# Optimization experiments

Measured on AMD Instinct MI355X. Metric: run time of the kernel, lower is better.

Reference implementation:

```python
import jax, jax.numpy as jnp
import numpy as np

B, CIN, H, W = 4, 272, 32, 32
D, NHEAD, DFF, E, TOPK, NDEC = 256, 8, 1024, 8, 2, 2
HW = H * W


def _sine_pos():
    npf = D // 2
    ye = jnp.cumsum(jnp.ones((H, W), jnp.float32), 0)
    xe = jnp.cumsum(jnp.ones((H, W), jnp.float32), 1)
    eps, scale = 1e-6, 2.0 * np.pi
    ye = ye / (ye[-1:, :] + eps) * scale
    xe = xe / (xe[:, -1:] + eps) * scale
    t = jnp.arange(npf, dtype=jnp.float32)
    dim_t = 10000.0 ** (2.0 * jnp.floor(t / 2.0) / npf)
    px = xe[:, :, None] / dim_t
    py = ye[:, :, None] / dim_t
    px = jnp.stack((jnp.sin(px[:, :, 0::2]), jnp.cos(px[:, :, 1::2])), axis=3).reshape(H, W, npf)
    py = jnp.stack((jnp.sin(py[:, :, 0::2]), jnp.cos(py[:, :, 1::2])), axis=3).reshape(H, W, npf)
    return jnp.concatenate((py, px), axis=2).reshape(HW, D)


def _ln(v, g, b):
    m = v.mean(-1, keepdims=True)
    var = ((v - m) ** 2).mean(-1, keepdims=True)
    return (v - m) / jnp.sqrt(var + 1e-5) * g + b


def _mha(q_in, k_in, v_in, Wqkv, bqkv, Wo, bo):
    # seq-first [S,B,D], torch nn.MultiheadAttention math (dropout off)
    S = q_in.shape[0]; T = k_in.shape[0]; dh = D // NHEAD
    Wq, Wk, Wv = jnp.split(Wqkv, 3, 0)
    bq, bk, bv = jnp.split(bqkv, 3)
    q = (q_in @ Wq.T + bq).reshape(S, B, NHEAD, dh)
    k = (k_in @ Wk.T + bk).reshape(T, B, NHEAD, dh)
    v = (v_in @ Wv.T + bv).reshape(T, B, NHEAD, dh)
    attn = jax.nn.softmax(jnp.einsum('sbhd,tbhd->bhst', q, k) / np.sqrt(dh), axis=-1)
    o = jnp.einsum('bhst,tbhd->sbhd', attn, v).reshape(S, B, D)
    return o @ Wo.T + bo


def _moe(xt, Wg, bg, W1, b1, W2, b2):
    # FMoETransformerMLP with NaiveGate: top-k gate, per-expert 2-layer MLP, weighted combine
    S = xt.shape[0]
    xf = xt.reshape(-1, D)
    N = xf.shape[0]
    logits = xf @ Wg.T + bg                              # [N, E]
    topv, topi = jax.lax.top_k(logits, TOPK)             # [N, k]
    score = jax.nn.softmax(topv, axis=-1)                # softmax over selected logits
    comb = jnp.zeros((N, E), xf.dtype).at[jnp.arange(N)[:, None], topi].add(score)
    h = jax.nn.relu(jnp.einsum('nd,edh->neh', xf, W1) + b1)   # [N, E, DFF]
    y = jnp.einsum('neh,ehd->ned', h, W2) + b2                # [N, E, D]
    out = jnp.einsum('ne,ned->nd', comb, y)
    return out.reshape(S, B, D)


def setup_inputs() -> dict:
    key = jax.random.key(0)
    ks = iter(jax.random.split(key, 32))
    g = lambda shp, s=0.02: s * jax.random.normal(next(ks), shp, jnp.float32)
    inp = {
        'x': jax.random.normal(next(ks), (B, CIN, H, W), jnp.float32),
        'Wi': g((D, CIN)), 'bi': jnp.zeros((D,), jnp.float32),
        'learned_embed': g((HW, D), 1.0),
        'Wqkv_s': g((3 * D, D)), 'bqkv_s': jnp.zeros((3 * D,), jnp.float32),
        'Wo_s': g((D, D)), 'bo_s': jnp.zeros((D,), jnp.float32),
        'Wqkv_c': g((3 * D, D)), 'bqkv_c': jnp.zeros((3 * D,), jnp.float32),
        'Wo_c': g((D, D)), 'bo_c': jnp.zeros((D,), jnp.float32),
        'ln_g': jnp.ones((4 * NDEC, D), jnp.float32), 'ln_b': jnp.zeros((4 * NDEC, D), jnp.float32),
        'gate_w1': g((E, D)), 'gate_b1': jnp.zeros((E,), jnp.float32),
        'W1a': g((E, D, DFF)), 'b1a': jnp.zeros((E, DFF), jnp.float32),
        'W2a': g((E, DFF, D)), 'b2a': jnp.zeros((E, D), jnp.float32),
        'gate_w2': g((E, D)), 'gate_b2': jnp.zeros((E,), jnp.float32),
        'W1b': g((E, D, DFF)), 'b1b': jnp.zeros((E, DFF), jnp.float32),
        'W2b': g((E, DFF, D)), 'b2b': jnp.zeros((E, D), jnp.float32),
        'Wout': g((CIN, D)), 'bout': jnp.zeros((CIN,), jnp.float32),
    }
    return inp


def reference(x, Wi, bi, learned_embed, Wqkv_s, bqkv_s, Wo_s, bo_s,
              Wqkv_c, bqkv_c, Wo_c, bo_c, ln_g, ln_b,
              gate_w1, gate_b1, W1a, b1a, W2a, b2a,
              gate_w2, gate_b2, W1b, b1b, W2b, b2b, Wout, bout):
    tokens = x.transpose(2, 3, 0, 1).reshape(HW, B, CIN)   # 'b c h w -> (h w) b c'
    src = tokens @ Wi.T + bi                               # input_proj
    pos = _sine_pos()[:, None, :]                          # [HW,1,D] broadcast over batch
    enc = src
    dec = src
    for i in range(NDEC):
        tgt = jnp.broadcast_to(learned_embed[:, None, :], (HW, B, D))
        t2 = _mha(tgt + pos, enc + pos, enc, Wqkv_s, bqkv_s, Wo_s, bo_s)
        tgt = _ln(tgt + t2, ln_g[4 * i], ln_b[4 * i])
        t2 = _mha(tgt + pos, dec + pos, dec, Wqkv_c, bqkv_c, Wo_c, bo_c)
        tgt = _ln(tgt + t2, ln_g[4 * i + 1], ln_b[4 * i + 1])
        od = tgt + _moe(tgt, gate_w1, gate_b1, W1a, b1a, W2a, b2a)   # post-lnorm: residual only
        od = _ln(od, ln_g[4 * i + 2], ln_b[4 * i + 2])
        od = od + _moe(od, gate_w2, gate_b2, W1b, b1b, W2b, b2b)
        dec = _ln(od, ln_g[4 * i + 3], ln_b[4 * i + 3])
    rec = dec @ Wout.T + bout                              # output_proj, [HW,B,CIN]
    feature_rec = rec.reshape(H, W, B, CIN).transpose(2, 3, 0, 1)
    return feature_rec
```

## Files before the change

### kernel.cpp

```cpp
#include <hip/hip_runtime.h>

#define NHW 1024
#define NB 4
#define DM 256
#define NTOK 4096
#define NCIN 272
#define NDFF 1024

typedef unsigned short u16;
typedef unsigned int u32;
typedef __attribute__((ext_vector_type(8))) short s16x8;
typedef __attribute__((ext_vector_type(4))) float f32x4;

static const int GEMM_SMEM32 = (32+32+64+64)*56*2;

__device__ __forceinline__ float4 ld4(const float* p){ return *(const float4*)p; }
__device__ __forceinline__ void st4(float* p, float4 v){ *(float4*)p = v; }

__device__ __forceinline__ void splitf(float x, u16& h, u16& l){
  u32 u = __float_as_uint(x);
  u32 hu = (u + (0x7FFFu + ((u >> 16) & 1u))) >> 16;
  h = (u16)hu;
  float hf = __uint_as_float(hu << 16);
  float r = x - hf;
  u32 v = __float_as_uint(r);
  v += 0x7FFFu + ((v >> 16) & 1u);
  l = (u16)(v >> 16);
}

__global__ void pos_kernel(float* __restrict__ pos){
  int s = blockIdx.x, d = threadIdx.x;
  int row = s >> 5, col = s & 31;
  float base = (d < 128) ? (float)(row + 1) : (float)(col + 1);
  float val = base / (32.0f + 1e-6f) * 6.2831853071795864f;
  int dd = (d < 128) ? d : d - 128;
  int mf = dd >> 1;
  float f = powf(10000.0f, (float)mf * (1.0f/64.0f));
  float a = val / f;
  pos[s*DM + d] = (dd & 1) ? cosf(a) : sinf(a);
}

__global__ void tin_kernel(const float* __restrict__ x, float* __restrict__ tok){
  int idx = blockIdx.x*256 + threadIdx.x;
  if (idx >= NTOK*NCIN) return;
  int c = idx % NCIN;
  int n = idx / NCIN;
  int s = n >> 2, b = n & 3;
  tok[idx] = x[((long)(b*NCIN + c))*NHW + s];
}
__global__ void tout_kernel(const float* __restrict__ rec, float* __restrict__ out){
  int idx = blockIdx.x*256 + threadIdx.x;
  if (idx >= NTOK*NCIN) return;
  int s = idx & (NHW-1);
  int bc = idx >> 10;
  int b = bc / NCIN, c = bc % NCIN;
  out[idx] = rec[((long)(s*NB + b))*NCIN + c];
}

__global__ __launch_bounds__(256) void tconv_kernel(const float* __restrict__ in,
    u16* __restrict__ oh, u16* __restrict__ ol, int K, int N){
  __shared__ float tile[32][33];
  long base = (long)blockIdx.z * (long)K * (long)N;
  int k0 = blockIdx.y*32, n0 = blockIdx.x*32;
  int tx = threadIdx.x & 31, ty = threadIdx.x >> 5;
  #pragma unroll
  for (int i=0;i<32;i+=8)
    tile[ty+i][tx] = in[base + (long)(k0+ty+i)*N + n0+tx];
  __syncthreads();
  #pragma unroll
  for (int i=0;i<32;i+=8){
    float v = tile[tx][ty+i];
    u16 h,l; splitf(v,h,l);
    long o = base + (long)(n0+ty+i)*K + k0+tx;
    oh[o]=h; ol[o]=l;
  }
}

__global__ void wsplit_kernel(const float* __restrict__ in, u16* __restrict__ oh,
    u16* __restrict__ ol, int n){
  int i = blockIdx.x*256 + threadIdx.x;
  if (i < n){ u16 h,l; splitf(in[i],h,l); oh[i]=h; ol[i]=l; }
}

template<bool GROUPED, bool INDIRECT, int ASRC, bool RELU, int CDST>
__device__ __forceinline__ void sgemm_body(
    const void* __restrict__ Av, int lda,
    const float* __restrict__ pos,
    const u16* __restrict__ Bhp, const u16* __restrict__ Blp, int ldb,
    const float* __restrict__ bias,
    void* __restrict__ Cv, int ldc,
    int M, int N, int K,
    const int* __restrict__ map,
    const int* __restrict__ cnt,
    const int* __restrict__ offs,
    const int* __restrict__ jmap,
    const float* __restrict__ sflat,
    long strideB, int strideBias, int e)
{
  constexpr int BM = 32;
  int rows = GROUPED ? cnt[e] : M;
  int bm = blockIdx.x, bn = blockIdx.y;
  if (bm*BM >= rows) return;
  int row0 = GROUPED ? offs[e] : 0;
  const float* Af = (const float*)Av;
  const u32*   Ap = (const u32*)Av;
  if (GROUPED){ Bhp += (long)e*strideB; Blp += (long)e*strideB; }
  const float* biasp = bias ? (GROUPED ? bias + (long)e*strideBias : bias) : nullptr;

  extern __shared__ u16 smem[];
  u16* Ah = smem;
  u16* Al = Ah + BM*56;
  u16* Bh = Al + BM*56;
  u16* Bl = Bh + 64*56;

  int tid = threadIdx.x;
  int w = tid >> 6, ln = tid & 63;
  int wm = w >> 1, wn = w & 1;
  int lr = ln & 15, lh = ln >> 4;
  int srow = tid >> 2, sseg = tid & 3;

  int bgrow = bn*64 + srow;
  bool bok = bgrow < N;
  int agrow = bm*BM + srow;
  bool aok = (tid < BM*4) && (agrow < rows);
  long arow = 0;
  if (aok) arow = INDIRECT ? (long)map[row0 + agrow] : (long)(row0 + agrow);

  const f32x4 z4 = {0.f,0.f,0.f,0.f};
  f32x4 acc0 = z4, acc1 = z4;
  const s16x8 z8 = {0,0,0,0,0,0,0,0};

  s16x8 rBh = z8, rBl = z8;
  uint4 rA0 = make_uint4(0,0,0,0), rA1 = make_uint4(0,0,0,0);
  float4 rP0 = make_float4(0.f,0.f,0.f,0.f), rP1 = rP0;

  auto load_stage = [&](int k0){
    int kk = k0 + sseg*8;
    bool kok = kk < K;
    rBh = z8; rBl = z8;
    if (bok && kok){
      rBh = *(const s16x8*)&Bhp[(long)bgrow*ldb + kk];
      rBl = *(const s16x8*)&Blp[(long)bgrow*ldb + kk];
    }
    if (tid < BM*4){
      rA0 = make_uint4(0,0,0,0); rA1 = make_uint4(0,0,0,0);
      if (ASRC==2 || ASRC==3){ rP0 = make_float4(0.f,0.f,0.f,0.f); rP1 = rP0; }
      if (aok && kok){
        if (ASRC == 1){
          rA0 = *(const uint4*)&Ap[arow*lda + kk];
          rA1 = *(const uint4*)&Ap[arow*lda + kk + 4];
        } else {
          long aoff = (ASRC==3 ? (long)(arow>>2) : arow)*lda + kk;
          rA0 = *(const uint4*)&Af[aoff];
          rA1 = *(const uint4*)&Af[aoff + 4];
          if (ASRC==2 || ASRC==3){
            long poff = (long)(arow>>2)*DM + kk;
            rP0 = ld4(&pos[poff]);
            rP1 = ld4(&pos[poff + 4]);
          }
        }
      }
    }
  };

  auto write_stage = [&](){
    *(s16x8*)&Bh[srow*56 + sseg*8] = rBh;
    *(s16x8*)&Bl[srow*56 + sseg*8] = rBl;
    if (tid < BM*4){
      s16x8 hv, lv;
      if (ASRC == 1){
        u32 ws[8] = {rA0.x,rA0.y,rA0.z,rA0.w,rA1.x,rA1.y,rA1.z,rA1.w};
        #pragma unroll
        for (int t=0;t<8;t++){ hv[t]=(short)(ws[t]&0xFFFFu); lv[t]=(short)(ws[t]>>16); }
      } else {
        float xs[8] = {__uint_as_float(rA0.x),__uint_as_float(rA0.y),
                       __uint_as_float(rA0.z),__uint_as_float(rA0.w),
                       __uint_as_float(rA1.x),__uint_as_float(rA1.y),
                       __uint_as_float(rA1.z),__uint_as_float(rA1.w)};
        if (ASRC==2 || ASRC==3){
          xs[0]+=rP0.x; xs[1]+=rP0.y; xs[2]+=rP0.z; xs[3]+=rP0.w;
          xs[4]+=rP1.x; xs[5]+=rP1.y; xs[6]+=rP1.z; xs[7]+=rP1.w;
        }
        #pragma unroll
        for (int t=0;t<8;t++){ u16 hh,ll; splitf(xs[t],hh,ll); hv[t]=(short)hh; lv[t]=(short)ll; }
      }
      *(s16x8*)&Ah[srow*56 + sseg*8] = hv;
      *(s16x8*)&Al[srow*56 + sseg*8] = lv;
    }
  };

  load_stage(0);
  for (int k0 = 0; k0 < K; k0 += 32){
    write_stage();
    __syncthreads();
    if (k0 + 32 < K) load_stage(k0 + 32);
    s16x8 a0h = *(const s16x8*)&Ah[(wm*16 + lr)*56 + lh*8];
    s16x8 a0l = *(const s16x8*)&Al[(wm*16 + lr)*56 + lh*8];
    s16x8 b0h = *(const s16x8*)&Bh[(wn*32      + lr)*56 + lh*8];
    s16x8 b1h = *(const s16x8*)&Bh[(wn*32 + 16 + lr)*56 + lh*8];
    s16x8 b0l = *(const s16x8*)&Bl[(wn*32      + lr)*56 + lh*8];
    s16x8 b1l = *(const s16x8*)&Bl[(wn*32 + 16 + lr)*56 + lh*8];
    acc0 = __builtin_amdgcn_mfma_f32_16x16x32_bf16(a0h, b0h, acc0, 0,0,0);
    acc1 = __builtin_amdgcn_mfma_f32_16x16x32_bf16(a0h, b1h, acc1, 0,0,0);
    acc0 = __builtin_amdgcn_mfma_f32_16x16x32_bf16(a0h, b0l, acc0, 0,0,0);
    acc1 = __builtin_amdgcn_mfma_f32_16x16x32_bf16(a0h, b1l, acc1, 0,0,0);
    acc0 = __builtin_amdgcn_mfma_f32_16x16x32_bf16(a0l, b0h, acc0, 0,0,0);
    acc1 = __builtin_amdgcn_mfma_f32_16x16x32_bf16(a0l, b1h, acc1, 0,0,0);
    __syncthreads();
  }

  int c0 = bn*64 + wn*32 + lr;
  int c1 = c0 + 16;
  float bv0 = (biasp && c0 < N) ? biasp[c0] : 0.f;
  float bv1 = (biasp && c1 < N) ? biasp[c1] : 0.f;
  int rbase = bm*BM + wm*16 + lh*4;
  auto stc = [&](int gr, int gc, float vv){
    if (gr < rows && gc < N){
      float t = RELU ? fmaxf(vv, 0.f) : vv;
      if (CDST == 1){
        u16 h,l; splitf(t,h,l);
        ((u32*)Cv)[(long)(row0+gr)*ldc + gc] = (u32)h | ((u32)l << 16);
      } else if (CDST == 2){
        int ts = jmap[row0+gr];
        ((float*)Cv)[(long)ts*ldc + gc] = t * sflat[ts];
      } else {
        ((float*)Cv)[(long)(row0+gr)*ldc + gc] = t;
      }
    }
  };
  #pragma unroll
  for (int r = 0; r < 4; r++){
    stc(rbase + r, c0, acc0[r] + bv0);
    stc(rbase + r, c1, acc1[r] + bv1);
  }
}

__global__ __launch_bounds__(256) void gemm_in(const float* A, const u16* Bh_, const u16* Bl_,
    const float* bias, float* C){
  sgemm_body<false,false,0,false,0>(A, NCIN, nullptr, Bh_, Bl_, NCIN, bias, C, DM,
      NTOK, DM, NCIN, nullptr, nullptr, nullptr, nullptr, nullptr, 0, 0, 0);
}

__global__ __launch_bounds__(256) void gemm_out_k(const float* A, const u16* Bh_, const u16* Bl_,
    const float* bias, float* C){
  sgemm_body<false,false,0,false,0>(A, DM, nullptr, Bh_, Bl_, DM, bias, C, NCIN,
      NTOK, NCIN, DM, nullptr, nullptr, nullptr, nullptr, nullptr, 0, 0, 0);
}

__global__ __launch_bounds__(256) void gemm_wos(const float* A, const u16* Bh_, const u16* Bl_,
    const float* bias, float* C){
  sgemm_body<false,false,0,false,0>(A, DM, nullptr, Bh_, Bl_, DM, bias, C, DM,
      NTOK, DM, DM, nullptr, nullptr, nullptr, nullptr, nullptr, 0, 0, 0);
}

__global__ __launch_bounds__(256) void gemm_woc(const float* A, const u16* Bh_, const u16* Bl_,
    const float* bias, float* C){
  sgemm_body<false,false,0,false,0>(A, DM, nullptr, Bh_, Bl_, DM, bias, C, DM,
      NTOK, DM, DM, nullptr, nullptr, nullptr, nullptr, nullptr, 0, 0, 0);
}

template<int MQ, int MK>
__device__ __forceinline__ void qkv_body(const float* Aq, const float* Ak, const float* Avv,
    const float* pos, const u16* Bwh, const u16* Bwl, const float* bias,
    float* Cq, float* Ck, float* Cvv){
  int z = blockIdx.z;
  const float* A = z==0 ? Aq : (z==1 ? Ak : Avv);
  float* C = z==0 ? Cq : (z==1 ? Ck : Cvv);
  const u16* Bph = Bwh + (long)z*256*DM;
  const u16* Bpl = Bwl + (long)z*256*DM;
  const float* bp = bias + z*256;
  int mode = z==0 ? MQ : (z==1 ? MK : 0);
  if (mode == 3)
    sgemm_body<false,false,3,false,0>(A, DM, pos, Bph, Bpl, DM, bp, C, DM,
        NTOK, DM, DM, nullptr, nullptr, nullptr, nullptr, nullptr, 0, 0, 0);
  else if (mode == 2)
    sgemm_body<false,false,2,false,0>(A, DM, pos, Bph, Bpl, DM, bp, C, DM,
        NTOK, DM, DM, nullptr, nullptr, nullptr, nullptr, nullptr, 0, 0, 0);
  else
    sgemm_body<false,false,0,false,0>(A, DM, pos, Bph, Bpl, DM, bp, C, DM,
        NTOK, DM, DM, nullptr, nullptr, nullptr, nullptr, nullptr, 0, 0, 0);
}

__global__ __launch_bounds__(256) void gemm_qkv_s(const float* Aq, const float* Ak,
    const float* Avv, const float* pos, const u16* Bwh, const u16* Bwl, const float* bias,
    float* Cq, float* Ck, float* Cvv){
  qkv_body<3,2>(Aq, Ak, Avv, pos, Bwh, Bwl, bias, Cq, Ck, Cvv);
}
__global__ __launch_bounds__(256) void gemm_qkv_c(const float* Aq, const float* Ak,
    const float* Avv, const float* pos, const u16* Bwh, const u16* Bwl, const float* bias,
    float* Cq, float* Ck, float* Cvv){
  qkv_body<2,2>(Aq, Ak, Avv, pos, Bwh, Bwl, bias, Cq, Ck, Cvv);
}

__global__ __launch_bounds__(256) void gemm_m1(const float* A, const u16* Bh_, const u16* Bl_,
    const float* bias, u32* C, const int* map, const int* cnt, const int* offs){
  sgemm_body<true,true,0,true,1>(A, DM, nullptr, Bh_, Bl_, DM, bias, C, NDFF,
      0, NDFF, DM, map, cnt, offs, nullptr, nullptr, 262144L, NDFF, blockIdx.z);
}

__global__ __launch_bounds__(256) void gemm_m2(const u32* A, const u16* Bh_, const u16* Bl_,
    const float* bias, float* C, const int* cnt, const int* offs,
    const int* jmap, const float* sflat){
  sgemm_body<true,false,1,false,2>(A, NDFF, nullptr, Bh_, Bl_, NDFF, bias, C, DM,
      0, DM, NDFF, nullptr, cnt, offs, jmap, sflat, 262144L, DM, blockIdx.z);
}

__global__ __launch_bounds__(256) void attn_mfma(const float* __restrict__ Q,
    const float* __restrict__ Kb, const float* __restrict__ Vb, float* __restrict__ O)
{
  __shared__ u16 Kh[64*40], Kl[64*40];
  __shared__ u16 Vh[32*72], Vl[32*72];
  __shared__ u16 Ph[4][16*72], Pl[4][16*72];

  int qt = blockIdx.x, bh = blockIdx.y;
  int b = bh >> 3, h = bh & 7;
  int tid = threadIdx.x;
  int wv = tid >> 6, ln = tid & 63;
  int lr = ln & 15, lh = ln >> 4;
  const float scale = 0.17677669529663687f;

  s16x8 qh, ql;
  {
    long qrow = ((long)((qt*64 + wv*16 + lr)*NB + b))*DM + h*32 + lh*8;
    float4 x0 = ld4(&Q[qrow]);
    float4 x1 = ld4(&Q[qrow + 4]);
    float xs[8] = {x0.x,x0.y,x0.z,x0.w,x1.x,x1.y,x1.z,x1.w};
    #pragma unroll
    for (int t=0;t<8;t++){
      u16 hh,ll; splitf(xs[t]*scale,hh,ll);
      qh[t]=(short)hh; ql[t]=(short)ll;
    }
  }

  const f32x4 z4 = {0.f,0.f,0.f,0.f};
  f32x4 oacc0 = z4, oacc1 = z4;
  float m[4]  = {-1e30f,-1e30f,-1e30f,-1e30f};
  float lp[4] = {0.f,0.f,0.f,0.f};

  for (int kt = 0; kt < 16; kt++){
    __syncthreads();
    {
      int key = tid >> 2, oct = tid & 3;
      long g = ((long)((kt*64 + key)*NB + b))*DM + h*32 + oct*8;
      float4 x0 = ld4(&Kb[g]);
      float4 x1 = ld4(&Kb[g + 4]);
      float xs[8] = {x0.x,x0.y,x0.z,x0.w,x1.x,x1.y,x1.z,x1.w};
      s16x8 hv, lv;
      #pragma unroll
      for (int t=0;t<8;t++){ u16 hh,ll; splitf(xs[t],hh,ll); hv[t]=(short)hh; lv[t]=(short)ll; }
      *(s16x8*)&Kh[key*40 + oct*8] = hv;
      *(s16x8*)&Kl[key*40 + oct*8] = lv;
    }
    #pragma unroll
    for (int it=0; it<2; it++){
      int idx = tid + it*256;
      int key = idx >> 3, d4 = (idx & 7) << 2;
      long g = ((long)((kt*64 + key)*NB + b))*DM + h*32 + d4;
      float4 x = ld4(&Vb[g]);
      u16 hh,ll;
      splitf(x.x,hh,ll); Vh[(d4+0)*72 + key]=hh; Vl[(d4+0)*72 + key]=ll;
      splitf(x.y,hh,ll); Vh[(d4+1)*72 + key]=hh; Vl[(d4+1)*72 + key]=ll;
      splitf(x.z,hh,ll); Vh[(d4+2)*72 + key]=hh; Vl[(d4+2)*72 + key]=ll;
      splitf(x.w,hh,ll); Vh[(d4+3)*72 + key]=hh; Vl[(d4+3)*72 + key]=ll;
    }
    __syncthreads();

    f32x4 sacc[4];
    #pragma unroll
    for (int s16t=0; s16t<4; s16t++){
      s16x8 kbh = *(const s16x8*)&Kh[(s16t*16 + lr)*40 + lh*8];
      s16x8 kbl = *(const s16x8*)&Kl[(s16t*16 + lr)*40 + lh*8];
      f32x4 a = z4;
      a = __builtin_amdgcn_mfma_f32_16x16x32_bf16(qh, kbh, a, 0,0,0);
      a = __builtin_amdgcn_mfma_f32_16x16x32_bf16(qh, kbl, a, 0,0,0);
      a = __builtin_amdgcn_mfma_f32_16x16x32_bf16(ql, kbh, a, 0,0,0);
      sacc[s16t] = a;
    }
    float tm[4];
    #pragma unroll
    for (int r=0;r<4;r++)
      tm[r] = fmaxf(fmaxf(sacc[0][r],sacc[1][r]), fmaxf(sacc[2][r],sacc[3][r]));
    #pragma unroll
    for (int mask=1; mask<=8; mask<<=1){
      #pragma unroll
      for (int r=0;r<4;r++) tm[r] = fmaxf(tm[r], __shfl_xor(tm[r], mask));
    }
    #pragma unroll
    for (int r=0;r<4;r++){
      float mn = fmaxf(m[r], tm[r]);
      float al = __expf(m[r] - mn);
      m[r] = mn;
      lp[r] *= al;
      oacc0[r] *= al;
      oacc1[r] *= al;
    }
    #pragma unroll
    for (int s16t=0; s16t<4; s16t++){
      #pragma unroll
      for (int r=0;r<4;r++){
        float p = __expf(sacc[s16t][r] - m[r]);
        lp[r] += p;
        u16 hh,ll; splitf(p,hh,ll);
        int off = (lh*4 + r)*72 + s16t*16 + lr;
        Ph[wv][off] = hh;
        Pl[wv][off] = ll;
      }
    }
    #pragma unroll
    for (int ks=0; ks<2; ks++){
      s16x8 pah = *(const s16x8*)&Ph[wv][lr*72 + ks*32 + lh*8];
      s16x8 pal = *(const s16x8*)&Pl[wv][lr*72 + ks*32 + lh*8];
      s16x8 vh0 = *(const s16x8*)&Vh[lr*72      + ks*32 + lh*8];
      s16x8 vl0 = *(const s16x8*)&Vl[lr*72      + ks*32 + lh*8];
      s16x8 vh1 = *(const s16x8*)&Vh[(16+lr)*72 + ks*32 + lh*8];
      s16x8 vl1 = *(const s16x8*)&Vl[(16+lr)*72 + ks*32 + lh*8];
      oacc0 = __builtin_amdgcn_mfma_f32_16x16x32_bf16(pah, vh0, oacc0, 0,0,0);
      oacc0 = __builtin_amdgcn_mfma_f32_16x16x32_bf16(pah, vl0, oacc0, 0,0,0);
      oacc0 = __builtin_amdgcn_mfma_f32_16x16x32_bf16(pal, vh0, oacc0, 0,0,0);
      oacc1 = __builtin_amdgcn_mfma_f32_16x16x32_bf16(pah, vh1, oacc1, 0,0,0);
      oacc1 = __builtin_amdgcn_mfma_f32_16x16x32_bf16(pah, vl1, oacc1, 0,0,0);
      oacc1 = __builtin_amdgcn_mfma_f32_16x16x32_bf16(pal, vh1, oacc1, 0,0,0);
    }
  }
  #pragma unroll
  for (int mask=1; mask<=8; mask<<=1){
    #pragma unroll
    for (int r=0;r<4;r++) lp[r] += __shfl_xor(lp[r], mask);
  }
  #pragma unroll
  for (int r=0;r<4;r++){
    float inv = 1.f/lp[r];
    int q = qt*64 + wv*16 + lh*4 + r;
    long orow = ((long)(q*NB + b))*DM + h*32;
    O[orow + lr]      = oacc0[r]*inv;
    O[orow + 16 + lr] = oacc1[r]*inv;
  }
}

__device__ __forceinline__ float wave_sum(float v){
  #pragma unroll
  for (int m=1; m<64; m<<=1) v += __shfl_xor(v, m);
  return v;
}

__device__ __forceinline__ float4 ln_finish(float4 a, const float* g, const float* beta, int lane){
  float sum = wave_sum(a.x+a.y+a.z+a.w);
  float sq  = wave_sum(a.x*a.x + a.y*a.y + a.z*a.z + a.w*a.w);
  float mean = sum * (1.f/DM);
  float var  = sq * (1.f/DM) - mean*mean;
  float inv = 1.0f / sqrtf(var + 1e-5f);
  float4 gg = ld4(&g[lane*4]);
  float4 bb = ld4(&beta[lane*4]);
  float4 ov;
  ov.x = (a.x-mean)*inv*gg.x + bb.x;
  ov.y = (a.y-mean)*inv*gg.y + bb.y;
  ov.z = (a.z-mean)*inv*gg.z + bb.z;
  ov.w = (a.w-mean)*inv*gg.w + bb.w;
  return ov;
}

__device__ __forceinline__ void gate_from_regs(float4 ov, int row, int lane,
    const float* GW, const float* GB, float* scores, int* topi){
  float lg[8];
  #pragma unroll
  for (int e=0; e<8; e++){
    float4 wv = ld4(&GW[e*DM + lane*4]);
    lg[e] = ov.x*wv.x + ov.y*wv.y + ov.z*wv.z + ov.w*wv.w;
  }
  #pragma unroll
  for (int mask=1; mask<64; mask<<=1){
    #pragma unroll
    for (int e=0; e<8; e++) lg[e] += __shfl_xor(lg[e], mask);
  }
  #pragma unroll
  for (int e=0; e<8; e++) lg[e] += GB[e];
  int i0 = 0; float v0 = lg[0];
  #pragma unroll
  for (int e=1; e<8; e++) if (lg[e] > v0){ v0 = lg[e]; i0 = e; }
  int i1 = -1; float v1 = -1e30f;
  #pragma unroll
  for (int e=0; e<8; e++) if (e != i0 && lg[e] > v1){ v1 = lg[e]; i1 = e; }
  if (lane == 0){
    float ee = expf(v1 - v0);
    float inv = 1.f/(1.f + ee);
    scores[row*2]   = inv;
    scores[row*2+1] = ee*inv;
    topi[row*2]   = i0;
    topi[row*2+1] = i1;
  }
}

__global__ __launch_bounds__(256) void add_ln_le(const float* __restrict__ A,
    const float* __restrict__ Bv, const float* __restrict__ g, const float* __restrict__ beta,
    float* __restrict__ out)
{
  int row = blockIdx.x*4 + (threadIdx.x >> 6);
  int lane = threadIdx.x & 63;
  float4 a = ld4(&A[(long)(row>>2)*DM + lane*4]);
  float4 b = ld4(&Bv[(long)row*DM + lane*4]);
  a.x+=b.x; a.y+=b.y; a.z+=b.z; a.w+=b.w;
  float4 ov = ln_finish(a, g, beta, lane);
  st4(&out[(long)row*DM + lane*4], ov);
}

__global__ __launch_bounds__(256) void add_ln_gate(const float* __restrict__ A,
    const float* __restrict__ Bv, const float* __restrict__ g, const float* __restrict__ beta,
    float* __restrict__ out, const float* __restrict__ GW, const float* __restrict__ GB,
    float* __restrict__ scores, int* __restrict__ topi)
{
  int row = blockIdx.x*4 + (threadIdx.x >> 6);
  int lane = threadIdx.x & 63;
  float4 a = ld4(&A[(long)row*DM + lane*4]);
  float4 b = ld4(&Bv[(long)row*DM + lane*4]);
  a.x+=b.x; a.y+=b.y; a.z+=b.z; a.w+=b.w;
  float4 ov = ln_finish(a, g, beta, lane);
  st4(&out[(long)row*DM + lane*4], ov);
  gate_from_regs(ov, row, lane, GW, GB, scores, topi);
}

__global__ __launch_bounds__(256) void moe_ln_gate_k(const float* __restrict__ base,
    const float* __restrict__ yt,
    const float* __restrict__ g, const float* __restrict__ beta, float* __restrict__ out,
    const float* __restrict__ GW, const float* __restrict__ GB,
    float* __restrict__ scores2, int* __restrict__ topi2)
{
  int row = blockIdx.x*4 + (threadIdx.x >> 6);
  int lane = threadIdx.x & 63;
  float4 a  = ld4(&base[(long)row*DM + lane*4]);
  float4 y0 = ld4(&yt[(long)(row*2)*DM + lane*4]);
  float4 y1 = ld4(&yt[(long)(row*2+1)*DM + lane*4]);
  a.x += y0.x + y1.x;
  a.y += y0.y + y1.y;
  a.z += y0.z + y1.z;
  a.w += y0.w + y1.w;
  float4 ov = ln_finish(a, g, beta, lane);
  st4(&out[(long)row*DM + lane*4], ov);
  gate_from_regs(ov, row, lane, GW, GB, scores2, topi2);
}

__global__ __launch_bounds__(256) void moe_ln_fin_k(const float* __restrict__ base,
    const float* __restrict__ yt,
    const float* __restrict__ g, const float* __restrict__ beta, float* __restrict__ out)
{
  int row = blockIdx.x*4 + (threadIdx.x >> 6);
  int lane = threadIdx.x & 63;
  float4 a  = ld4(&base[(long)row*DM + lane*4]);
  float4 y0 = ld4(&yt[(long)(row*2)*DM + lane*4]);
  float4 y1 = ld4(&yt[(long)(row*2+1)*DM + lane*4]);
  a.x += y0.x + y1.x;
  a.y += y0.y + y1.y;
  a.z += y0.z + y1.z;
  a.w += y0.w + y1.w;
  float4 ov = ln_finish(a, g, beta, lane);
  st4(&out[(long)row*DM + lane*4], ov);
}

__global__ void offs_assign(const int* __restrict__ topi, int* __restrict__ cnt_g,
    int* __restrict__ offs_g, int* __restrict__ map, int* __restrict__ jmap)
{
  __shared__ int hist[72];
  __shared__ int offs[8];
  __shared__ int c2[8];
  int tid = threadIdx.x;
  if (tid < 72) hist[tid] = 0;
  __syncthreads();
  for (int idx = tid; idx < 2*NTOK; idx += 256){
    int e = topi[idx];
    atomicAdd(&hist[e*9 + (tid & 7)], 1);
  }
  __syncthreads();
  if (tid == 0){
    int o = 0;
    #pragma unroll
    for (int e=0; e<8; e++){
      int c = 0;
      #pragma unroll
      for (int s=0; s<8; s++) c += hist[e*9 + s];
      cnt_g[e] = c;
      offs[e] = o;
      offs_g[e] = o;
      o += c;
      c2[e] = 0;
    }
  }
  __syncthreads();
  for (int n = tid; n < NTOK; n += 256){
    #pragma unroll
    for (int j=0; j<2; j++){
      int e = topi[n*2+j];
      int slot = atomicAdd(&c2[e], 1);
      int r = offs[e] + slot;
      map[r] = n;
      jmap[r] = n*2 + j;
    }
  }
}

extern "C" void kernel_launch(void* const* d_in, const int* in_sizes, int n_in,
                              void* d_out, int out_size, void* d_ws, size_t ws_size,
                              hipStream_t stream)
{
  const float* x      = (const float*)d_in[0];
  const float* Wi     = (const float*)d_in[1];
  const float* bi     = (const float*)d_in[2];
  const float* le     = (const float*)d_in[3];
  const float* Wqkv_s = (const float*)d_in[4];
  const float* bqkv_s = (const float*)d_in[5];
  const float* Wo_s   = (const float*)d_in[6];
  const float* bo_s   = (const float*)d_in[7];
  const float* Wqkv_c = (const float*)d_in[8];
  const float* bqkv_c = (const float*)d_in[9];
  const float* Wo_c   = (const float*)d_in[10];
  const float* bo_c   = (const float*)d_in[11];
  const float* ln_g   = (const float*)d_in[12];
  const float* ln_b   = (const float*)d_in[13];
  const float* gw1    = (const float*)d_in[14];
  const float* gb1    = (const float*)d_in[15];
  const float* W1a    = (const float*)d_in[16];
  const float* b1a    = (const float*)d_in[17];
  const float* W2a    = (const float*)d_in[18];
  const float* b2a    = (const float*)d_in[19];
  const float* gw2    = (const float*)d_in[20];
  const float* gb2    = (const float*)d_in[21];
  const float* W1b    = (const float*)d_in[22];
  const float* b1b    = (const float*)d_in[23];
  const float* W2b    = (const float*)d_in[24];
  const float* b2b    = (const float*)d_in[25];
  const float* Wout   = (const float*)d_in[26];
  const float* bout   = (const float*)d_in[27];

  float* w = (float*)d_ws;
  const long SZ = 1048576;
  float* pos  = w;
  float* src  = pos  + 262144;
  float* t2s  = src  + SZ;
  float* tgtA = t2s  + SZ;
  float* dec  = tgtA + SZ;
  float* od   = dec;
  float* od2  = dec  + SZ;
  float* yt   = od2  + SZ;
  float* scoresA = yt + 2097152;
  float* scoresB = scoresA + 8192;
  u16* wsp  = (u16*)(scoresB + 8192);
  u16* W1ah = wsp;             u16* W1al = wsp + 2097152;
  u16* W1bh = wsp + 4194304;   u16* W1bl = wsp + 6291456;
  u16* W2ah = wsp + 8388608;   u16* W2al = wsp + 10485760;
  u16* W2bh = wsp + 12582912;  u16* W2bl = wsp + 14680064;
  u16* dwp  = wsp + 16777216;
  u16* Wih   = dwp;            u16* Wil   = dwp + 69632;
  u16* Wqsh  = dwp + 139264;   u16* Wqsl  = dwp + 335872;
  u16* Wosh  = dwp + 532480;   u16* Wosl  = dwp + 598016;
  u16* Wqch  = dwp + 663552;   u16* Wqcl  = dwp + 860160;
  u16* Woch  = dwp + 1056768;  u16* Wocl  = dwp + 1122304;
  u16* Wouth = dwp + 1187840;  u16* Woutl = dwp + 1257472;
  float* R   = (float*)(dwp + 1327104);
  float* tok = R;
  float* q   = R;
  float* k   = R + SZ;
  float* v   = R + 2*SZ;
  float* ao  = R + 3*SZ;
  u32*  hg   = (u32*)R;
  float* rec = R;
  int* ip    = (int*)(R + 8388608);
  int* topiA = ip;
  int* topiB = ip + 8192;
  int* map   = ip + 16384;
  int* jmapA = ip + 24576;
  int* jmapB = ip + 32768;
  int* cnts  = ip + 40960;
  int* offsg = ip + 40992;

  dim3 blk(256);
  dim3 gDense(128, 4, 1);
  dim3 gQKV(128, 4, 3);
  dim3 gMoe1(128, 16, 8);
  dim3 gMoe2(128, 4, 8);
  dim3 gAttn(16, 32);

  pos_kernel<<<NHW, DM, 0, stream>>>(pos);
  tin_kernel<<<(NTOK*NCIN + 255)/256, blk, 0, stream>>>(x, tok);

  tconv_kernel<<<dim3(32, 8, 8), blk, 0, stream>>>(W1a, W1ah, W1al, DM,   NDFF);
  tconv_kernel<<<dim3(32, 8, 8), blk, 0, stream>>>(W1b, W1bh, W1bl, DM,   NDFF);
  tconv_kernel<<<dim3(8, 32, 8), blk, 0, stream>>>(W2a, W2ah, W2al, NDFF, DM);
  tconv_kernel<<<dim3(8, 32, 8), blk, 0, stream>>>(W2b, W2bh, W2bl, NDFF, DM);
  wsplit_kernel<<<272, blk, 0, stream>>>(Wi,     Wih,   Wil,   69632);
  wsplit_kernel<<<768, blk, 0, stream>>>(Wqkv_s, Wqsh,  Wqsl,  196608);
  wsplit_kernel<<<256, blk, 0, stream>>>(Wo_s,   Wosh,  Wosl,  65536);
  wsplit_kernel<<<768, blk, 0, stream>>>(Wqkv_c, Wqch,  Wqcl,  196608);
  wsplit_kernel<<<256, blk, 0, stream>>>(Wo_c,   Woch,  Wocl,  65536);
  wsplit_kernel<<<272, blk, 0, stream>>>(Wout,   Wouth, Woutl, 69632);

  gemm_in<<<gDense, blk, GEMM_SMEM32, stream>>>(tok, Wih, Wil, bi, src);

  gemm_qkv_s<<<gQKV, blk, GEMM_SMEM32, stream>>>(le, src, src, pos, Wqsh, Wqsl, bqkv_s, q, k, v);
  attn_mfma<<<gAttn, blk, 0, stream>>>(q, k, v, ao);
  gemm_wos<<<gDense, blk, GEMM_SMEM32, stream>>>(ao, Wosh, Wosl, bo_s, t2s);

  const float* decIn = src;
  for (int i = 0; i < 2; i++){
    int* cntA = cnts + (i*2)*8;   int* offsA = offsg + (i*2)*8;
    int* cntB = cnts + (i*2+1)*8; int* offsB = offsg + (i*2+1)*8;

    add_ln_le<<<1024, blk, 0, stream>>>(le, t2s, ln_g + (4*i)*DM, ln_b + (4*i)*DM, tgtA);
    gemm_qkv_c<<<gQKV, blk, GEMM_SMEM32, stream>>>(tgtA, decIn, decIn, pos, Wqch, Wqcl, bqkv_c, q, k, v);
    attn_mfma<<<gAttn, blk, 0, stream>>>(q, k, v, ao);
    gemm_woc<<<gDense, blk, GEMM_SMEM32, stream>>>(ao, Woch, Wocl, bo_c, k);
    add_ln_gate<<<1024, blk, 0, stream>>>(tgtA, k, ln_g + (4*i+1)*DM, ln_b + (4*i+1)*DM, od,
        gw1, gb1, scoresA, topiA);

    offs_assign<<<1, blk, 0, stream>>>(topiA, cntA, offsA, map, jmapA);
    gemm_m1<<<gMoe1, blk, GEMM_SMEM32, stream>>>(od, W1ah, W1al, b1a, hg, map, cntA, offsA);
    gemm_m2<<<gMoe2, blk, GEMM_SMEM32, stream>>>(hg, W2ah, W2al, b2a, yt, cntA, offsA,
        jmapA, scoresA);
    moe_ln_gate_k<<<1024, blk, 0, stream>>>(od, yt,
        ln_g + (4*i+2)*DM, ln_b + (4*i+2)*DM, od2, gw2, gb2, scoresB, topiB);

    offs_assign<<<1, blk, 0, stream>>>(topiB, cntB, offsB, map, jmapB);
    gemm_m1<<<gMoe1, blk, GEMM_SMEM32, stream>>>(od2, W1bh, W1bl, b1b, hg, map, cntB, offsB);
    gemm_m2<<<gMoe2, blk, GEMM_SMEM32, stream>>>(hg, W2bh, W2bl, b2b, yt, cntB, offsB,
        jmapB, scoresB);
    moe_ln_fin_k<<<1024, blk, 0, stream>>>(od2, yt,
        ln_g + (4*i+3)*DM, ln_b + (4*i+3)*DM, dec);

    decIn = dec;
  }

  gemm_out_k<<<dim3(128,5,1), blk, GEMM_SMEM32, stream>>>(dec, Wouth, Woutl, bout, rec);
  tout_kernel<<<(NTOK*NCIN + 255)/256, blk, 0, stream>>>(rec, (float*)d_out);
}
```

Before: 742.2 us.

## Store QKV and attention outputs pre-split as packed bf16 hi/lo pairs

The QKV projection GEMMs and the attention kernel now write their outputs as packed bf16 hi/lo words instead of fp32. Downstream consumers (attention K/V/Q loads and the Wo GEMMs) unpack them directly and no longer run the split routine. The softmax scale moves from Q preprocessing to the score accumulators. This removes repeated split work inside the attention inner loop, which splits each K/V tile once per query tile, at the cost of changing the interface of several kernels.

Result: no change. 730.6 us (-1.6%).

```diff
diff --git a/kernel.cpp b/kernel.cpp
--- a/kernel.cpp
+++ b/kernel.cpp
@@ -26,6 +26,11 @@
   u32 v = __float_as_uint(r);
   v += 0x7FFFu + ((v >> 16) & 1u);
   l = (u16)(v >> 16);
+}
+
+__device__ __forceinline__ u32 packf(float x){
+  u16 h,l; splitf(x,h,l);
+  return (u32)h | ((u32)l << 16);
 }
 
 __global__ void pos_kernel(float* __restrict__ pos){
@@ -218,8 +223,7 @@
     if (gr < rows && gc < N){
       float t = RELU ? fmaxf(vv, 0.f) : vv;
       if (CDST == 1){
-        u16 h,l; splitf(t,h,l);
-        ((u32*)Cv)[(long)(row0+gr)*ldc + gc] = (u32)h | ((u32)l << 16);
+        ((u32*)Cv)[(long)(row0+gr)*ldc + gc] = packf(t);
       } else if (CDST == 2){
         int ts = jmap[row0+gr];
         ((float*)Cv)[(long)ts*ldc + gc] = t * sflat[ts];
@@ -247,48 +251,48 @@
       NTOK, NCIN, DM, nullptr, nullptr, nullptr, nullptr, nullptr, 0, 0, 0);
 }
 
-__global__ __launch_bounds__(256) void gemm_wos(const float* A, const u16* Bh_, const u16* Bl_,
+__global__ __launch_bounds__(256) void gemm_wos(const u32* A, const u16* Bh_, const u16* Bl_,
     const float* bias, float* C){
-  sgemm_body<false,false,0,false,0>(A, DM, nullptr, Bh_, Bl_, DM, bias, C, DM,
+  sgemm_body<false,false,1,false,0>(A, DM, nullptr, Bh_, Bl_, DM, bias, C, DM,
       NTOK, DM, DM, nullptr, nullptr, nullptr, nullptr, nullptr, 0, 0, 0);
 }
 
-__global__ __launch_bounds__(256) void gemm_woc(const float* A, const u16* Bh_, const u16* Bl_,
+__global__ __launch_bounds__(256) void gemm_woc(const u32* A, const u16* Bh_, const u16* Bl_,
     const float* bias, float* C){
-  sgemm_body<false,false,0,false,0>(A, DM, nullptr, Bh_, Bl_, DM, bias, C, DM,
+  sgemm_body<false,false,1,false,0>(A, DM, nullptr, Bh_, Bl_, DM, bias, C, DM,
       NTOK, DM, DM, nullptr, nullptr, nullptr, nullptr, nullptr, 0, 0, 0);
 }
 
 template<int MQ, int MK>
 __device__ __forceinline__ void qkv_body(const float* Aq, const float* Ak, const float* Avv,
     const float* pos, const u16* Bwh, const u16* Bwl, const float* bias,
-    float* Cq, float* Ck, float* Cvv){
+    u32* Cq, u32* Ck, u32* Cvv){
   int z = blockIdx.z;
   const float* A = z==0 ? Aq : (z==1 ? Ak : Avv);
-  float* C = z==0 ? Cq : (z==1 ? Ck : Cvv);
+  u32* C = z==0 ? Cq : (z==1 ? Ck : Cvv);
   const u16* Bph = Bwh + (long)z*256*DM;
   const u16* Bpl = Bwl + (long)z*256*DM;
   const float* bp = bias + z*256;
   int mode = z==0 ? MQ : (z==1 ? MK : 0);
   if (mode == 3)
-    sgemm_body<false,false,3,false,0>(A, DM, pos, Bph, Bpl, DM, bp, C, DM,
+    sgemm_body<false,false,3,false,1>(A, DM, pos, Bph, Bpl, DM, bp, C, DM,
         NTOK, DM, DM, nullptr, nullptr, nullptr, nullptr, nullptr, 0, 0, 0);
   else if (mode == 2)
-    sgemm_body<false,false,2,false,0>(A, DM, pos, Bph, Bpl, DM, bp, C, DM,
+    sgemm_body<false,false,2,false,1>(A, DM, pos, Bph, Bpl, DM, bp, C, DM,
         NTOK, DM, DM, nullptr, nullptr, nullptr, nullptr, nullptr, 0, 0, 0);
   else
-    sgemm_body<false,false,0,false,0>(A, DM, pos, Bph, Bpl, DM, bp, C, DM,
+    sgemm_body<false,false,0,false,1>(A, DM, pos, Bph, Bpl, DM, bp, C, DM,
         NTOK, DM, DM, nullptr, nullptr, nullptr, nullptr, nullptr, 0, 0, 0);
 }
 
 __global__ __launch_bounds__(256) void gemm_qkv_s(const float* Aq, const float* Ak,
     const float* Avv, const float* pos, const u16* Bwh, const u16* Bwl, const float* bias,
-    float* Cq, float* Ck, float* Cvv){
+    u32* Cq, u32* Ck, u32* Cvv){
   qkv_body<3,2>(Aq, Ak, Avv, pos, Bwh, Bwl, bias, Cq, Ck, Cvv);
 }
 __global__ __launch_bounds__(256) void gemm_qkv_c(const float* Aq, const float* Ak,
     const float* Avv, const float* pos, const u16* Bwh, const u16* Bwl, const float* bias,
-    float* Cq, float* Ck, float* Cvv){
+    u32* Cq, u32* Ck, u32* Cvv){
   qkv_body<2,2>(Aq, Ak, Avv, pos, Bwh, Bwl, bias, Cq, Ck, Cvv);
 }
 
@@ -305,8 +309,8 @@
       0, DM, NDFF, nullptr, cnt, offs, jmap, sflat, 262144L, DM, blockIdx.z);
 }
 
-__global__ __launch_bounds__(256) void attn_mfma(const float* __restrict__ Q,
-    const float* __restrict__ Kb, const float* __restrict__ Vb, float* __restrict__ O)
+__global__ __launch_bounds__(256) void attn_mfma(const u32* __restrict__ Q,
+    const u32* __restrict__ Kb, const u32* __restrict__ Vb, u32* __restrict__ O)
 {
   __shared__ u16 Kh[64*40], Kl[64*40];
   __shared__ u16 Vh[32*72], Vl[32*72];
@@ -322,14 +326,11 @@
   s16x8 qh, ql;
   {
     long qrow = ((long)((qt*64 + wv*16 + lr)*NB + b))*DM + h*32 + lh*8;
-    float4 x0 = ld4(&Q[qrow]);
-    float4 x1 = ld4(&Q[qrow + 4]);
-    float xs[8] = {x0.x,x0.y,x0.z,x0.w,x1.x,x1.y,x1.z,x1.w};
-    #pragma unroll
-    for (int t=0;t<8;t++){
-      u16 hh,ll; splitf(xs[t]*scale,hh,ll);
-      qh[t]=(short)hh; ql[t]=(short)ll;
-    }
+    uint4 p0 = *(const uint4*)&Q[qrow];
+    uint4 p1 = *(const uint4*)&Q[qrow + 4];
+    u32 ws[8] = {p0.x,p0.y,p0.z,p0.w,p1.x,p1.y,p1.z,p1.w};
+    #pragma unroll
+    for (int t=0;t<8;t++){ qh[t]=(short)(ws[t]&0xFFFFu); ql[t]=(short)(ws[t]>>16); }
   }
 
   const f32x4 z4 = {0.f,0.f,0.f,0.f};
@@ -342,12 +343,12 @@
     {
       int key = tid >> 2, oct = tid & 3;
       long g = ((long)((kt*64 + key)*NB + b))*DM + h*32 + oct*8;
-      float4 x0 = ld4(&Kb[g]);
-      float4 x1 = ld4(&Kb[g + 4]);
-      float xs[8] = {x0.x,x0.y,x0.z,x0.w,x1.x,x1.y,x1.z,x1.w};
+      uint4 x0 = *(const uint4*)&Kb[g];
+      uint4 x1 = *(const uint4*)&Kb[g + 4];
+      u32 ws[8] = {x0.x,x0.y,x0.z,x0.w,x1.x,x1.y,x1.z,x1.w};
       s16x8 hv, lv;
       #pragma unroll
-      for (int t=0;t<8;t++){ u16 hh,ll; splitf(xs[t],hh,ll); hv[t]=(short)hh; lv[t]=(short)ll; }
+      for (int t=0;t<8;t++){ hv[t]=(short)(ws[t]&0xFFFFu); lv[t]=(short)(ws[t]>>16); }
       *(s16x8*)&Kh[key*40 + oct*8] = hv;
       *(s16x8*)&Kl[key*40 + oct*8] = lv;
     }
@@ -356,12 +357,13 @@
       int idx = tid + it*256;
       int key = idx >> 3, d4 = (idx & 7) << 2;
       long g = ((long)((kt*64 + key)*NB + b))*DM + h*32 + d4;
-      float4 x = ld4(&Vb[g]);
-      u16 hh,ll;
-      splitf(x.x,hh,ll); Vh[(d4+0)*72 + key]=hh; Vl[(d4+0)*72 + key]=ll;
-      splitf(x.y,hh,ll); Vh[(d4+1)*72 + key]=hh; Vl[(d4+1)*72 + key]=ll;
-      splitf(x.z,hh,ll); Vh[(d4+2)*72 + key]=hh; Vl[(d4+2)*72 + key]=ll;
-      splitf(x.w,hh,ll); Vh[(d4+3)*72 + key]=hh; Vl[(d4+3)*72 + key]=ll;
+      uint4 x = *(const uint4*)&Vb[g];
+      u32 ws[4] = {x.x,x.y,x.z,x.w};
+      #pragma unroll
+      for (int t=0;t<4;t++){
+        Vh[(d4+t)*72 + key] = (u16)(ws[t]&0xFFFFu);
+        Vl[(d4+t)*72 + key] = (u16)(ws[t]>>16);
+      }
     }
     __syncthreads();
 
@@ -374,6 +376,7 @@
       a = __builtin_amdgcn_mfma_f32_16x16x32_bf16(qh, kbh, a, 0,0,0);
       a = __builtin_amdgcn_mfma_f32_16x16x32_bf16(qh, kbl, a, 0,0,0);
       a = __builtin_amdgcn_mfma_f32_16x16x32_bf16(ql, kbh, a, 0,0,0);
+      a[0]*=scale; a[1]*=scale; a[2]*=scale; a[3]*=scale;
       sacc[s16t] = a;
     }
     float tm[4];
@@ -432,8 +435,8 @@
     float inv = 1.f/lp[r];
     int q = qt*64 + wv*16 + lh*4 + r;
     long orow = ((long)(q*NB + b))*DM + h*32;
-    O[orow + lr]      = oacc0[r]*inv;
-    O[orow + 16 + lr] = oacc1[r]*inv;
+    O[orow + lr]      = packf(oacc0[r]*inv);
+    O[orow + 16 + lr] = packf(oacc1[r]*inv);
   }
 }
 
@@ -655,10 +658,10 @@
   u16* Wouth = dwp + 1187840;  u16* Woutl = dwp + 1257472;
   float* R   = (float*)(dwp + 1327104);
   float* tok = R;
-  float* q   = R;
-  float* k   = R + SZ;
-  float* v   = R + 2*SZ;
-  float* ao  = R + 3*SZ;
+  u32*  q    = (u32*)R;
+  u32*  k    = (u32*)(R + SZ);
+  u32*  v    = (u32*)(R + 2*SZ);
+  u32*  ao   = (u32*)(R + 3*SZ);
   u32*  hg   = (u32*)R;
   float* rec = R;
   int* ip    = (int*)(R + 8388608);
@@ -705,8 +708,8 @@
     add_ln_le<<<1024, blk, 0, stream>>>(le, t2s, ln_g + (4*i)*DM, ln_b + (4*i)*DM, tgtA);
     gemm_qkv_c<<<gQKV, blk, GEMM_SMEM32, stream>>>(tgtA, decIn, decIn, pos, Wqch, Wqcl, bqkv_c, q, k, v);
     attn_mfma<<<gAttn, blk, 0, stream>>>(q, k, v, ao);
-    gemm_woc<<<gDense, blk, GEMM_SMEM32, stream>>>(ao, Woch, Wocl, bo_c, k);
-    add_ln_gate<<<1024, blk, 0, stream>>>(tgtA, k, ln_g + (4*i+1)*DM, ln_b + (4*i+1)*DM, od,
+    gemm_woc<<<gDense, blk, GEMM_SMEM32, stream>>>(ao, Woch, Wocl, bo_c, (float*)k);
+    add_ln_gate<<<1024, blk, 0, stream>>>(tgtA, (float*)k, ln_g + (4*i+1)*DM, ln_b + (4*i+1)*DM, od,
         gw1, gb1, scoresA, topiA);
 
     offs_assign<<<1, blk, 0, stream>>>(topiA, cntA, offsA, map, jmapA);
```
